# Performance work log

Hardware: AMD Instinct MI355X
Metric: run time of the kernel (lower is better)

Reference implementation:

```python
import jax, jax.numpy as jnp
import numpy as np

BATCH, WIDTH, HEIGHT, DEPTH = 1024, 256, 256, 8


def setup_inputs() -> dict:
    key = jax.random.key(0)
    k_val, k_m1, k_b1, k_m2, k_b2 = jax.random.split(key, 5)
    return {
        "val": jax.random.normal(k_val, (BATCH, 1), dtype=jnp.float32),
        "M1": jax.random.normal(k_m1, (DEPTH, WIDTH, HEIGHT), dtype=jnp.float32),
        "B1": jax.random.normal(k_b1, (DEPTH, WIDTH, HEIGHT), dtype=jnp.float32),
        "M2": jax.random.normal(k_m2, (DEPTH, WIDTH, HEIGHT), dtype=jnp.float32),
        "B2": jax.random.normal(k_b2, (DEPTH, WIDTH, HEIGHT), dtype=jnp.float32),
    }


def _run_branch(q0, M, B):
    # q0: [B]; M, B: [depth, W, H]. Sequential recurrence over depth.
    def step(q, mb):
        m, b = mb  # [W, H]
        s = q[:, None, None] * m[None] + b[None]        # [B, W, H]
        q_new = jnp.min(jnp.max(s, axis=-1), axis=-1)    # max over H, then min over W -> [B]
        return q_new, None

    q_final, _ = jax.lax.scan(step, q0, (M, B))
    return q_final


def reference(val, M1, B1, M2, B2):
    q0 = val[:, 0]  # val: [B, 1] -> [B]
    q1 = _run_branch(q0, M1, B1)
    q2 = _run_branch(q0, M2, B2)
    return q1[:, None], q2[:, None]  # each [B, 1], matching torch squeeze(-1) of [B,1,1]
```

## Files before the change

kernel.cpp:

```cpp
#include <hip/hip_runtime.h>
#include <math.h>

#define WH     256
#define NDEPTH 8
#define NBATCH 1024
#define NB     8
#define PLANE  (WH * WH)

typedef _Float16 h2 __attribute__((ext_vector_type(2)));

#define HQBLK  (NDEPTH * 64 * WH)

__global__ __launch_bounds__(256) void transpose_half_k(const float* __restrict__ M1,
                                                        const float* __restrict__ B1,
                                                        const float* __restrict__ M2,
                                                        const float* __restrict__ B2,
                                                        _Float16* __restrict__ wsh) {
    __shared__ float tile[64][65];
    const int bid = blockIdx.x;
    const int arr = bid >> 7;
    const int d   = (bid >> 4) & 7;
    const int ht  = (bid >> 2) & 3;
    const int wt  = bid & 3;

    const float* src = (arr == 0) ? M1 : (arr == 1) ? B1 : (arr == 2) ? M2 : B2;
    const float* s = src + d * PLANE;
    _Float16* o = wsh + ((size_t)(arr * 4 + ht) * NDEPTH + d) * (64 * WH);

    const int t   = threadIdx.x;
    const int q16 = t >> 4;
    const int r16 = t & 15;

#pragma unroll
    for (int p = 0; p < 4; ++p) {
        const int wrow = q16 + p * 16;
        const float4 v = *(const float4*)(s + (wt * 64 + wrow) * WH + ht * 64 + r16 * 4);
        tile[wrow][r16 * 4 + 0] = v.x;
        tile[wrow][r16 * 4 + 1] = v.y;
        tile[wrow][r16 * 4 + 2] = v.z;
        tile[wrow][r16 * 4 + 3] = v.w;
    }
    __syncthreads();
#pragma unroll
    for (int p = 0; p < 4; ++p) {
        const int hrow = q16 + p * 16;
        const int wl   = r16 * 4;
        union { _Float16 f[4]; uint2 u; } pk;
        pk.f[0] = (_Float16)tile[wl + 0][hrow];
        pk.f[1] = (_Float16)tile[wl + 1][hrow];
        pk.f[2] = (_Float16)tile[wl + 2][hrow];
        pk.f[3] = (_Float16)tile[wl + 3][hrow];
        *(uint2*)(o + hrow * WH + wt * 64 + wl) = pk.u;
    }
}

__global__ __launch_bounds__(256) void prop_h_k(const _Float16* __restrict__ wsh,
                                                const float* __restrict__ val,
                                                float* __restrict__ out) {
    const int bid  = blockIdx.x;
    const int x    = bid & 7;
    const int br   = x >> 2;
    const int bg   = (bid >> 3) * 4 + (x & 3);
    const int t    = threadIdx.x;
    const int wave = t >> 6;
    const int lane = t & 63;

    const int arrM = br ? 2 : 0;
    const int arrB = br ? 3 : 1;
    const uint4* __restrict__ mp = (const uint4*)wsh + (size_t)(arrM * 4 + wave) * (HQBLK / 8) + lane;
    const uint4* __restrict__ bp = (const uint4*)wsh + (size_t)(arrB * 4 + wave) * (HQBLK / 8) + lane;

    h2 q2[NB];
#pragma unroll
    for (int nb = 0; nb < NB; ++nb) {
        const _Float16 qh = (_Float16)val[bg * NB + nb];
        q2[nb].x = qh; q2[nb].y = qh;
    }

    __shared__ h2 part[8][NB][128];
    __shared__ float qs[NB];

    union H8 { uint4 u; h2 h[4]; };

    uint4 bm[4][2], bb[4][2];
#pragma unroll
    for (int s = 0; s < 3; ++s) {
        bm[s][0] = mp[0]; bm[s][1] = mp[64];
        bb[s][0] = bp[0]; bb[s][1] = bp[64];
        mp += 128; bp += 128;
    }

    union { unsigned short us; _Float16 f; } ninf; ninf.us = 0xFC00;
    h2 NEGINF; NEGINF.x = ninf.f; NEGINF.y = ninf.f;

    for (int d = 0; d < NDEPTH; ++d) {
        h2 acc[NB][4];
#pragma unroll
        for (int nb = 0; nb < NB; ++nb)
#pragma unroll
            for (int k = 0; k < 4; ++k) acc[nb][k] = NEGINF;

#pragma unroll
        for (int c = 0; c < 16; ++c) {
            const int slot = c & 3;
            const int ps   = (c + 3) & 3;
            bm[ps][0] = mp[0]; bm[ps][1] = mp[64];
            bb[ps][0] = bp[0]; bb[ps][1] = bp[64];
            mp += 128; bp += 128;

            H8 m0, m1, b0, b1;
            m0.u = bm[slot][0]; m1.u = bm[slot][1];
            b0.u = bb[slot][0]; b1.u = bb[slot][1];
#pragma unroll
            for (int nb = 0; nb < NB; ++nb) {
                const h2 qq = q2[nb];
#pragma unroll
                for (int k = 0; k < 4; ++k) {
                    acc[nb][k] = __builtin_elementwise_max(
                        acc[nb][k], __builtin_elementwise_fma(qq, m0.h[k], b0.h[k]));
                    acc[nb][k] = __builtin_elementwise_max(
                        acc[nb][k], __builtin_elementwise_fma(qq, m1.h[k], b1.h[k]));
                }
            }
        }

        const int vw  = wave * 2 + (lane >> 5);
        const int j32 = lane & 31;
#pragma unroll
        for (int nb = 0; nb < NB; ++nb) {
            H8 st;
            st.h[0] = acc[nb][0]; st.h[1] = acc[nb][1];
            st.h[2] = acc[nb][2]; st.h[3] = acc[nb][3];
            *(uint4*)&part[vw][nb][j32 * 4] = st.u;
        }
        __syncthreads();

        {
            const int nb = t >> 5;
            const int j  = t & 31;
            H8 v; v.u = *(const uint4*)&part[0][nb][j * 4];
#pragma unroll
            for (int s2 = 1; s2 < 8; ++s2) {
                H8 w2; w2.u = *(const uint4*)&part[s2][nb][j * 4];
#pragma unroll
                for (int k = 0; k < 4; ++k)
                    v.h[k] = __builtin_elementwise_max(v.h[k], w2.h[k]);
            }
            h2 mn = __builtin_elementwise_min(
                        __builtin_elementwise_min(v.h[0], v.h[1]),
                        __builtin_elementwise_min(v.h[2], v.h[3]));
            float r = fminf((float)mn.x, (float)mn.y);
#pragma unroll
            for (int off = 16; off > 0; off >>= 1)
                r = fminf(r, __shfl_xor(r, off, 32));
            if (j == 0) qs[nb] = r;
        }
        __syncthreads();
#pragma unroll
        for (int nb = 0; nb < NB; ++nb) {
            const _Float16 qh = (_Float16)qs[nb];
            q2[nb].x = qh; q2[nb].y = qh;
        }
    }

    if (t < NB) out[br * NBATCH + bg * NB + t] = qs[t];
}

extern "C" void kernel_launch(void* const* d_in, const int* in_sizes, int n_in,
                              void* d_out, int out_size, void* d_ws, size_t ws_size,
                              hipStream_t stream) {
    const float* val = (const float*)d_in[0];
    const float* M1  = (const float*)d_in[1];
    const float* B1  = (const float*)d_in[2];
    const float* M2  = (const float*)d_in[3];
    const float* B2  = (const float*)d_in[4];
    float*    out = (float*)d_out;
    _Float16* wsh = (_Float16*)d_ws;

    transpose_half_k<<<dim3(512), dim3(256), 0, stream>>>(M1, B1, M2, B2, wsh);
    prop_h_k<<<dim3(256), dim3(256), 0, stream>>>(wsh, val, out);
}
```

Measured before the change: 113.9 us.

## Split H dimension across 8 waves per block instead of 4

Rearranges the transposed half-precision workspace into eight 32-row H slices and launches the propagation kernel with 512 threads, so each wave processes half as many H rows per depth step. Within each wave the two half-wave partial maxima are combined with a cross-lane shuffle before the LDS reduction. The aim is more waves per CU to hide load latency and shorten the serial per-wave work. In exchange it adds shuffle overhead and a larger block-wide barrier at every depth step.

After: 115.0 us. No clear change (+0.9%).

```diff
diff --git a/kernel.cpp b/kernel.cpp
--- a/kernel.cpp
+++ b/kernel.cpp
@@ -9,7 +9,7 @@
 
 typedef _Float16 h2 __attribute__((ext_vector_type(2)));
 
-#define HQBLK  (NDEPTH * 64 * WH)
+#define HOBLK  (NDEPTH * 32 * WH)
 
 __global__ __launch_bounds__(256) void transpose_half_k(const float* __restrict__ M1,
                                                         const float* __restrict__ B1,
@@ -25,7 +25,6 @@
 
     const float* src = (arr == 0) ? M1 : (arr == 1) ? B1 : (arr == 2) ? M2 : B2;
     const float* s = src + d * PLANE;
-    _Float16* o = wsh + ((size_t)(arr * 4 + ht) * NDEPTH + d) * (64 * WH);
 
     const int t   = threadIdx.x;
     const int q16 = t >> 4;
@@ -44,17 +43,21 @@
 #pragma unroll
     for (int p = 0; p < 4; ++p) {
         const int hrow = q16 + p * 16;
+        const int ho   = ht * 2 + (hrow >> 5);
+        const int hs   = hrow & 31;
         const int wl   = r16 * 4;
+        _Float16* o = wsh + ((size_t)(arr * 8 + ho) * NDEPTH + d) * (32 * WH)
+                          + hs * WH + wt * 64 + wl;
         union { _Float16 f[4]; uint2 u; } pk;
         pk.f[0] = (_Float16)tile[wl + 0][hrow];
         pk.f[1] = (_Float16)tile[wl + 1][hrow];
         pk.f[2] = (_Float16)tile[wl + 2][hrow];
         pk.f[3] = (_Float16)tile[wl + 3][hrow];
-        *(uint2*)(o + hrow * WH + wt * 64 + wl) = pk.u;
+        *(uint2*)o = pk.u;
     }
 }
 
-__global__ __launch_bounds__(256) void prop_h_k(const _Float16* __restrict__ wsh,
+__global__ __launch_bounds__(512) void prop_h_k(const _Float16* __restrict__ wsh,
                                                 const float* __restrict__ val,
                                                 float* __restrict__ out) {
     const int bid  = blockIdx.x;
@@ -67,8 +70,8 @@
 
     const int arrM = br ? 2 : 0;
     const int arrB = br ? 3 : 1;
-    const uint4* __restrict__ mp = (const uint4*)wsh + (size_t)(arrM * 4 + wave) * (HQBLK / 8) + lane;
-    const uint4* __restrict__ bp = (const uint4*)wsh + (size_t)(arrB * 4 + wave) * (HQBLK / 8) + lane;
+    const uint4* __restrict__ mp = (const uint4*)wsh + (size_t)(arrM * 8 + wave) * (HOBLK / 8) + lane;
+    const uint4* __restrict__ bp = (const uint4*)wsh + (size_t)(arrB * 8 + wave) * (HOBLK / 8) + lane;
 
     h2 q2[NB];
 #pragma unroll
@@ -82,12 +85,11 @@
 
     union H8 { uint4 u; h2 h[4]; };
 
-    uint4 bm[4][2], bb[4][2];
+    uint4 bm[4], bb[4];
 #pragma unroll
     for (int s = 0; s < 3; ++s) {
-        bm[s][0] = mp[0]; bm[s][1] = mp[64];
-        bb[s][0] = bp[0]; bb[s][1] = bp[64];
-        mp += 128; bp += 128;
+        bm[s] = mp[0]; bb[s] = bp[0];
+        mp += 64; bp += 64;
     }
 
     union { unsigned short us; _Float16 f; } ninf; ninf.us = 0xFC00;
@@ -104,13 +106,11 @@
         for (int c = 0; c < 16; ++c) {
             const int slot = c & 3;
             const int ps   = (c + 3) & 3;
-            bm[ps][0] = mp[0]; bm[ps][1] = mp[64];
-            bb[ps][0] = bp[0]; bb[ps][1] = bp[64];
-            mp += 128; bp += 128;
+            bm[ps] = mp[0]; bb[ps] = bp[0];
+            mp += 64; bp += 64;
 
-            H8 m0, m1, b0, b1;
-            m0.u = bm[slot][0]; m1.u = bm[slot][1];
-            b0.u = bb[slot][0]; b1.u = bb[slot][1];
+            H8 m0, b0;
+            m0.u = bm[slot]; b0.u = bb[slot];
 #pragma unroll
             for (int nb = 0; nb < NB; ++nb) {
                 const h2 qq = q2[nb];
@@ -118,24 +118,33 @@
                 for (int k = 0; k < 4; ++k) {
                     acc[nb][k] = __builtin_elementwise_max(
                         acc[nb][k], __builtin_elementwise_fma(qq, m0.h[k], b0.h[k]));
-                    acc[nb][k] = __builtin_elementwise_max(
-                        acc[nb][k], __builtin_elementwise_fma(qq, m1.h[k], b1.h[k]));
                 }
             }
         }
 
-        const int vw  = wave * 2 + (lane >> 5);
-        const int j32 = lane & 31;
 #pragma unroll
-        for (int nb = 0; nb < NB; ++nb) {
-            H8 st;
-            st.h[0] = acc[nb][0]; st.h[1] = acc[nb][1];
-            st.h[2] = acc[nb][2]; st.h[3] = acc[nb][3];
-            *(uint4*)&part[vw][nb][j32 * 4] = st.u;
+        for (int nb = 0; nb < NB; ++nb)
+#pragma unroll
+            for (int k = 0; k < 4; ++k) {
+                const int av = __builtin_bit_cast(int, acc[nb][k]);
+                const int ov = __shfl_xor(av, 32, 64);
+                const h2 other = __builtin_bit_cast(h2, ov);
+                acc[nb][k] = __builtin_elementwise_max(acc[nb][k], other);
+            }
+
+        if (lane < 32) {
+            const int j32 = lane & 31;
+#pragma unroll
+            for (int nb = 0; nb < NB; ++nb) {
+                H8 st;
+                st.h[0] = acc[nb][0]; st.h[1] = acc[nb][1];
+                st.h[2] = acc[nb][2]; st.h[3] = acc[nb][3];
+                *(uint4*)&part[wave][nb][j32 * 4] = st.u;
+            }
         }
         __syncthreads();
 
-        {
+        if (t < 256) {
             const int nb = t >> 5;
             const int j  = t & 31;
             H8 v; v.u = *(const uint4*)&part[0][nb][j * 4];
@@ -178,5 +187,5 @@
     _Float16* wsh = (_Float16*)d_ws;
 
     transpose_half_k<<<dim3(512), dim3(256), 0, stream>>>(M1, B1, M2, B2, wsh);
-    prop_h_k<<<dim3(256), dim3(256), 0, stream>>>(wsh, val, out);
+    prop_h_k<<<dim3(256), dim3(512), 0, stream>>>(wsh, val, out);
 }
```
